# Kernel optimization log

Measured on AMD Instinct MI355X. Metric: run time of the kernel, lower is better.

## Reference

```python
import jax, jax.numpy as jnp
import numpy as np

B, H, P, L = 8, 512, 512, 2048
HIGH_STAB, LOW_STAB = 0.9, 0.99  # 0 <= high < |lambda| <= low <= 1 (discrete dynamics)


def setup_inputs() -> dict:
    key = jax.random.key(0)
    k_u, k_mag, k_ph, k_b, k_c, k_d = jax.random.split(key, 6)
    u = jax.random.normal(k_u, (B, H, L), dtype=jnp.float32)
    # Frozen diagonal reservoir state matrix Lambda_bar: complex eigenvalues with
    # magnitude in (high_stability, low_stability], random phase (stored as real/imag pairs).
    mag = jax.random.uniform(k_mag, (P,), minval=HIGH_STAB, maxval=LOW_STAB)
    phase = jax.random.uniform(k_ph, (P,), minval=0.0, maxval=2.0 * np.pi)
    Lambda_bar_ri = jnp.stack([mag * jnp.cos(phase), mag * jnp.sin(phase)], axis=-1)  # (P,2)
    B_bar_ri = jax.random.normal(k_b, (P, H, 2), dtype=jnp.float32)  # complex B_bar as real pairs
    C_ri = jax.random.normal(k_c, (H, P, 2), dtype=jnp.float32)      # complex C as real pairs
    D = jax.random.normal(k_d, (H, H), dtype=jnp.float32)
    return {"u": u, "Lambda_bar_ri": Lambda_bar_ri, "B_bar_ri": B_bar_ri, "C_ri": C_ri, "D": D}


def _binary_op(e_i, e_j):
    A_i, Bu_i = e_i
    A_j, Bu_j = e_j
    return (A_j * A_i, A_j * Bu_i + Bu_j)


def reference(u, Lambda_bar_ri, B_bar_ri, C_ri, D):
    Lam = jax.lax.complex(Lambda_bar_ri[:, 0], Lambda_bar_ri[:, 1])        # (P,)
    B_bar = jax.lax.complex(B_bar_ri[..., 0], B_bar_ri[..., 1])            # (P,H)
    C = jax.lax.complex(C_ri[..., 0], C_ri[..., 1])                        # (H,P)
    # Bu_t = B_bar @ u_t for all t, batched: (B,P,L) complex
    Bu = jnp.einsum('ph,bhl->bpl', B_bar, u.astype(B_bar.dtype))
    A = jnp.broadcast_to(Lam[None, :, None], Bu.shape)                     # (B,P,L)
    # Parallel associative scan: x_t = Lam * x_{t-1} + Bu_t
    _, x = jax.lax.associative_scan(_binary_op, (A, Bu), axis=2)           # (B,P,L)
    C_A_Bu = jnp.einsum('hp,bpl->bhl', C, x).real                          # (B,H,L)
    # torch.einsum('hh,bhl->bhl', D, u) uses only the diagonal of D
    Du = jnp.diagonal(D)[None, :, None] * u
    return jax.nn.gelu(C_A_Bu + Du, approximate=False)
```

## Files before the change

### kernel.cpp

```cpp
#include <hip/hip_runtime.h>
#include <cstdint>
#include <cstddef>

#define BB 8
#define HH 512
#define PP 512
#define LL 2048

typedef __attribute__((ext_vector_type(8))) __bf16 bf16x8;
typedef __attribute__((ext_vector_type(4))) float f32x4;

__device__ __forceinline__ uint16_t f2bf(float f) {
  uint32_t u = __builtin_bit_cast(uint32_t, f);
  u += 0x7FFFu + ((u >> 16) & 1u);
  return (uint16_t)(u >> 16);
}

__device__ __forceinline__ void async_copy16(const void* gptr, void* ldsptr) {
  __builtin_amdgcn_global_load_lds(
      (const __attribute__((address_space(1))) unsigned int*)gptr,
      (__attribute__((address_space(3))) unsigned int*)ldsptr,
      16, 0, 0);
}

__global__ __launch_bounds__(256) void prep_and_transpose(
    const float* __restrict__ U, const float* __restrict__ Bbar,
    const float* __restrict__ Cri, const float* __restrict__ Dm,
    uint16_t* __restrict__ Ut, uint16_t* __restrict__ A1,
    uint16_t* __restrict__ A2, float* __restrict__ Dd) {
  __shared__ uint16_t tile[64][66];
  const int t = threadIdx.x;
  if (blockIdx.x < 2048) {
    const int bid = blockIdx.x;
    const int b = bid >> 8;
    const int h0 = ((bid >> 5) & 7) * 64;
    const int l0 = (bid & 31) * 64;
    const int r = t >> 2, c = t & 3;
    const float* src = U + ((size_t)(b * 512 + h0 + r)) * 2048 + l0 + c * 16;
#pragma unroll
    for (int q = 0; q < 4; ++q) {
      float4 v = *(const float4*)(src + q * 4);
      *(uint32_t*)&tile[r][c * 16 + q * 4]     = (uint32_t)f2bf(v.x) | ((uint32_t)f2bf(v.y) << 16);
      *(uint32_t*)&tile[r][c * 16 + q * 4 + 2] = (uint32_t)f2bf(v.z) | ((uint32_t)f2bf(v.w) << 16);
    }
    __syncthreads();
    uint16_t* dst = Ut + ((size_t)(b * 2048 + l0 + r)) * 512 + h0 + c * 16;
    uint32_t o[8];
#pragma unroll
    for (int k = 0; k < 8; ++k)
      o[k] = (uint32_t)tile[c * 16 + 2 * k][r] | ((uint32_t)tile[c * 16 + 2 * k + 1][r] << 16);
    *(uint4*)(dst)     = make_uint4(o[0], o[1], o[2], o[3]);
    *(uint4*)(dst + 8) = make_uint4(o[4], o[5], o[6], o[7]);
  } else {
    int idx = (blockIdx.x - 2048) * 256 + t;
    int p = idx >> 9, h = idx & 511;
    A1[(size_t)p * 512 + h]          = f2bf(Bbar[((size_t)p * 512 + h) * 2 + 0]);
    A1[(size_t)(512 + p) * 512 + h]  = f2bf(Bbar[((size_t)p * 512 + h) * 2 + 1]);
    int h2 = idx >> 9, p2 = idx & 511;
    A2[(size_t)h2 * 1024 + p2]        = f2bf( Cri[((size_t)h2 * 512 + p2) * 2 + 0]);
    A2[(size_t)h2 * 1024 + 512 + p2]  = f2bf(-Cri[((size_t)h2 * 512 + p2) * 2 + 1]);
    if (idx < 512) Dd[idx] = Dm[(size_t)idx * 512 + idx];
  }
}

__global__ __launch_bounds__(512) void scan_tr(
    const float* __restrict__ Lam, const uint16_t* __restrict__ Bu,
    uint16_t* __restrict__ Xt8) {
  __shared__ uint16_t S[16][2048];
  const int t = threadIdx.x, wave = t >> 6, lane = t & 63;
  const int b = blockIdx.x >> 6, p0 = (blockIdx.x & 63) * 8, p = p0 + wave;

  const float lr = Lam[p * 2 + 0], li = Lam[p * 2 + 1];
  float ar = lr, ai = li;
#pragma unroll
  for (int s = 0; s < 5; ++s) { float nr = ar * ar - ai * ai, ni = 2.f * ar * ai; ar = nr; ai = ni; }

  const uint16_t* rowre = Bu + ((size_t)(b * 1024 + p)) * 2048 + lane * 32;
  const uint16_t* rowim = Bu + ((size_t)(b * 1024 + 512 + p)) * 2048 + lane * 32;
  uint4 vr[4], vi[4];
#pragma unroll
  for (int q = 0; q < 4; ++q) { vr[q] = ((const uint4*)rowre)[q]; vi[q] = ((const uint4*)rowim)[q]; }

  float xr[32], xi[32];
  float sr = 0.f, si = 0.f;
#pragma unroll
  for (int q = 0; q < 4; ++q) {
    uint32_t wr[4] = {vr[q].x, vr[q].y, vr[q].z, vr[q].w};
    uint32_t wi[4] = {vi[q].x, vi[q].y, vi[q].z, vi[q].w};
#pragma unroll
    for (int d = 0; d < 4; ++d) {
      float br0 = __builtin_bit_cast(float, wr[d] << 16);
      float bi0 = __builtin_bit_cast(float, wi[d] << 16);
      float br1 = __builtin_bit_cast(float, wr[d] & 0xFFFF0000u);
      float bi1 = __builtin_bit_cast(float, wi[d] & 0xFFFF0000u);
      int j = q * 8 + d * 2;
      float nr = lr * sr - li * si + br0, ni = lr * si + li * sr + bi0;
      sr = nr; si = ni; xr[j] = sr; xi[j] = si;
      nr = lr * sr - li * si + br1; ni = lr * si + li * sr + bi1;
      sr = nr; si = ni; xr[j + 1] = sr; xi[j + 1] = si;
    }
  }
  float Ar = ar, Ai = ai, Sr = sr, Si = si;
#pragma unroll
  for (int off = 1; off < 64; off <<= 1) {
    float pAr = __shfl_up(Ar, off), pAi = __shfl_up(Ai, off);
    float pSr = __shfl_up(Sr, off), pSi = __shfl_up(Si, off);
    if (lane >= off) {
      float tSr = Ar * pSr - Ai * pSi + Sr;
      float tSi = Ar * pSi + Ai * pSr + Si;
      float tAr = Ar * pAr - Ai * pAi;
      float tAi = Ar * pAi + Ai * pAr;
      Sr = tSr; Si = tSi; Ar = tAr; Ai = tAi;
    }
  }
  float Cr = __shfl_up(Sr, 1), Ci = __shfl_up(Si, 1);
  if (lane == 0) { Cr = 0.f; Ci = 0.f; }
  float fr_ = lr * Cr - li * Ci, fi_ = lr * Ci + li * Cr;
#pragma unroll
  for (int j = 0; j < 32; ++j) {
    xr[j] += fr_; xi[j] += fi_;
    float nfr = fr_ * lr - fi_ * li, nfi = fr_ * li + fi_ * lr;
    fr_ = nfr; fi_ = nfi;
  }
  const int wsw = (lane & 7) << 3;
#pragma unroll
  for (int q = 0; q < 4; ++q) {
    uint32_t wr[4], wi[4];
#pragma unroll
    for (int d = 0; d < 4; ++d) {
      int j = q * 8 + d * 2;
      wr[d] = (uint32_t)f2bf(xr[j]) | ((uint32_t)f2bf(xr[j + 1]) << 16);
      wi[d] = (uint32_t)f2bf(xi[j]) | ((uint32_t)f2bf(xi[j + 1]) << 16);
    }
    const int col = (lane * 32 + q * 8) ^ wsw;
    *(uint4*)&S[wave * 2 + 0][col] = make_uint4(wr[0], wr[1], wr[2], wr[3]);
    *(uint4*)&S[wave * 2 + 1][col] = make_uint4(wi[0], wi[1], wi[2], wi[3]);
  }
  __syncthreads();
  const size_t gre = (size_t)b * 128 + (p0 >> 3);
#pragma unroll
  for (int c = 0; c < 2; ++c) {
    uint16_t* dst = Xt8 + (gre + (size_t)c * 64) * 2048 * 8;
#pragma unroll
    for (int rep = 0; rep < 4; ++rep) {
      int l = rep * 512 + t;
      int ls = l ^ (((l >> 5) & 7) << 3);
      uint32_t o0 = (uint32_t)S[0 + c][ls] | ((uint32_t)S[2 + c][ls] << 16);
      uint32_t o1 = (uint32_t)S[4 + c][ls] | ((uint32_t)S[6 + c][ls] << 16);
      uint32_t o2 = (uint32_t)S[8 + c][ls] | ((uint32_t)S[10 + c][ls] << 16);
      uint32_t o3 = (uint32_t)S[12 + c][ls] | ((uint32_t)S[14 + c][ls] << 16);
      *(uint4*)(dst + (size_t)l * 8) = make_uint4(o0, o1, o2, o3);
    }
  }
}

#define GEMM_SETUP(KDIM, PB0_EXPR)                                            \
  constexpr int K = (KDIM), NT = K / 32;                                      \
  const int t = threadIdx.x, lane = t & 63, w = t >> 6;                       \
  const int m0 = blockIdx.y * 128, n0 = blockIdx.x * 64, b = blockIdx.z;      \
  const int r0 = t >> 2;                                                      \
  const int c0 = (t & 3) ^ ((r0 >> 1) & 3);                                   \
  const uint16_t* pA0 = Amat + (size_t)(m0 + r0) * K + c0 * 8;                \
  const uint16_t* pA1 = Amat + (size_t)(m0 + 64 + r0) * K + c0 * 8;           \
  const uint16_t* pB0 = (PB0_EXPR);                                           \
  const int d0 = t * 8;                                                       \
  const int wm = (w >> 1) * 64, wn = (w & 1) * 32;                            \
  const int fr = lane & 15, fq = lane >> 4;                                   \
  int offA[4], offB[2];                                                       \
  _Pragma("unroll")                                                           \
  for (int i = 0; i < 4; ++i) {                                               \
    int rm = wm + i * 16 + fr;                                                \
    offA[i] = rm * 32 + ((fq ^ ((rm >> 1) & 3)) * 8);                         \
  }                                                                           \
  _Pragma("unroll")                                                           \
  for (int j = 0; j < 2; ++j) {                                               \
    int rn = wn + j * 16 + fr;                                                \
    offB[j] = rn * 32 + ((fq ^ ((rn >> 1) & 3)) * 8);                         \
  }                                                                           \
  f32x4 acc[4][2];                                                            \
  _Pragma("unroll")                                                           \
  for (int i = 0; i < 4; ++i)                                                 \
    _Pragma("unroll")                                                         \
    for (int j = 0; j < 2; ++j) acc[i][j] = (f32x4){0.f, 0.f, 0.f, 0.f};

#define GEMM_MFMA_BLOCK(BUF_A, BUF_B)                                         \
  {                                                                           \
    bf16x8 af[4], bv[2];                                                      \
    _Pragma("unroll")                                                         \
    for (int i = 0; i < 4; ++i) af[i] = *(const bf16x8*)&(BUF_A)[offA[i]];    \
    _Pragma("unroll")                                                         \
    for (int j = 0; j < 2; ++j) bv[j] = *(const bf16x8*)&(BUF_B)[offB[j]];    \
    _Pragma("unroll")                                                         \
    for (int i = 0; i < 4; ++i)                                               \
      _Pragma("unroll")                                                       \
      for (int j = 0; j < 2; ++j)                                             \
        acc[i][j] = __builtin_amdgcn_mfma_f32_16x16x32_bf16(af[i], bv[j], acc[i][j], 0, 0, 0); \
  }

__global__ __launch_bounds__(256) void gemm1_fused(
    const uint16_t* __restrict__ Amat, const uint16_t* __restrict__ Bt,
    uint16_t* __restrict__ Bu) {
  __shared__ __align__(16) uint16_t Alds[2][128 * 32];
  __shared__ __align__(16) uint16_t Blds[2][64 * 32];
  GEMM_SETUP(512, Bt + ((size_t)b * 2048 + n0 + r0) * 512 + c0 * 8)
  async_copy16(pA0, &Alds[0][d0]);
  async_copy16(pA1, &Alds[0][2048 + d0]);
  async_copy16(pB0, &Blds[0][d0]);
  __syncthreads();
#pragma unroll 2
  for (int it = 0; it < NT; ++it) {
    const int cur = it & 1, nxt = cur ^ 1;
    if (it + 1 < NT) {
      const int kb = (it + 1) * 32;
      async_copy16(pA0 + kb, &Alds[nxt][d0]);
      async_copy16(pA1 + kb, &Alds[nxt][2048 + d0]);
      async_copy16(pB0 + kb, &Blds[nxt][d0]);
    }
    GEMM_MFMA_BLOCK(Alds[cur], Blds[cur])
    __syncthreads();
  }
  uint16_t* O = Bu + ((size_t)b * 1024 + m0) * 2048 + n0;
#pragma unroll
  for (int i = 0; i < 4; ++i)
#pragma unroll
    for (int j = 0; j < 2; ++j)
#pragma unroll
      for (int r = 0; r < 4; ++r) {
        int mm = wm + i * 16 + fq * 4 + r;
        int nn = wn + j * 16 + fr;
        O[(size_t)mm * 2048 + nn] = f2bf(acc[i][j][r]);
      }
}

__global__ __launch_bounds__(256) void gemm2_fused(
    const uint16_t* __restrict__ Amat, const uint16_t* __restrict__ Bt,
    float* __restrict__ Out, const float* __restrict__ Dd,
    const float* __restrict__ Uu) {
  __shared__ __align__(16) uint16_t Alds[3][128 * 32];
  __shared__ __align__(16) uint16_t Blds[3][64 * 32];
  GEMM_SETUP(1024, Bt + (((size_t)b * 128 + c0) * 2048 + n0 + r0) * 8)
  constexpr size_t BSTRIDE = 65536;
  async_copy16(pA0,           &Alds[0][d0]);
  async_copy16(pA1,           &Alds[0][2048 + d0]);
  async_copy16(pB0,           &Blds[0][d0]);
  async_copy16(pA0 + 32,      &Alds[1][d0]);
  async_copy16(pA1 + 32,      &Alds[1][2048 + d0]);
  async_copy16(pB0 + BSTRIDE, &Blds[1][d0]);
#pragma unroll
  for (int kt = 0; kt < NT; ++kt) {
    const int cur = kt % 3;
    if (kt + 1 < NT) asm volatile("s_waitcnt vmcnt(3)" ::: "memory");
    else             asm volatile("s_waitcnt vmcnt(0)" ::: "memory");
    __builtin_amdgcn_s_barrier();
    __builtin_amdgcn_sched_barrier(0);
    if (kt + 2 < NT) {
      const int nb = (kt + 2) % 3;
      const int kb = (kt + 2) * 32;
      async_copy16(pA0 + kb, &Alds[nb][d0]);
      async_copy16(pA1 + kb, &Alds[nb][2048 + d0]);
      async_copy16(pB0 + (size_t)(kt + 2) * BSTRIDE, &Blds[nb][d0]);
    }
    GEMM_MFMA_BLOCK(Alds[cur], Blds[cur])
  }
  const size_t base = ((size_t)b * 512 + m0) * 2048 + n0;
  float* O = Out + base;
  const float* Ub = Uu + base;
#pragma unroll
  for (int i = 0; i < 4; ++i)
#pragma unroll
    for (int r = 0; r < 4; ++r) {
      int mm = wm + i * 16 + fq * 4 + r;
      float dv = Dd[m0 + mm];
#pragma unroll
      for (int j = 0; j < 2; ++j) {
        int nn = wn + j * 16 + fr;
        float xv = acc[i][j][r] + dv * Ub[(size_t)mm * 2048 + nn];
        O[(size_t)mm * 2048 + nn] = 0.5f * xv * (1.f + erff(xv * 0.70710678118654752f));
      }
    }
}

extern "C" void kernel_launch(void* const* d_in, const int* in_sizes, int n_in,
                              void* d_out, int out_size, void* d_ws, size_t ws_size,
                              hipStream_t stream) {
  const float* u    = (const float*)d_in[0];
  const float* Lam  = (const float*)d_in[1];
  const float* Bbar = (const float*)d_in[2];
  const float* Cri  = (const float*)d_in[3];
  const float* Dm   = (const float*)d_in[4];
  float* out = (float*)d_out;

  char* ws = (char*)d_ws;
  uint16_t* Bu  = (uint16_t*)(ws);
  uint16_t* Xt8 = (uint16_t*)(ws + 33554432);
  uint16_t* Ut  = (uint16_t*)(ws + 33554432);
  uint16_t* A1 = (uint16_t*)(ws + 67108864);
  uint16_t* A2 = (uint16_t*)(ws + 68157440);
  float*    Dd = (float*)   (ws + 69206016);

  prep_and_transpose<<<3072, 256, 0, stream>>>(u, Bbar, Cri, Dm, Ut, A1, A2, Dd);
  gemm1_fused<<<dim3(32, 8, BB), 256, 0, stream>>>(A1, Ut, Bu);
  scan_tr<<<512, 512, 0, stream>>>(Lam, Bu, Xt8);
  gemm2_fused<<<dim3(32, 4, BB), 256, 0, stream>>>(A2, Xt8, out, Dd, u);
}
```

Baseline: 174.4 us.

## Fuse u transpose and bf16 conversion into gemm1 B-tile loading

Removes the separate transpose kernel that converted u to a bf16 (B,L,H) buffer. gemm1 now reads fp32 u directly with float4 loads, converts it to bf16 and writes it into the swizzled B tile in LDS, so the intermediate Ut write and read are gone. The cost is synchronous global loads plus conversion inside the main loop in place of async LDS copies, and u is reread for each of the 8 M-blocks.

```diff
diff --git a/kernel.cpp b/kernel.cpp
--- a/kernel.cpp
+++ b/kernel.cpp
@@ -23,44 +23,19 @@
       16, 0, 0);
 }
 
-__global__ __launch_bounds__(256) void prep_and_transpose(
-    const float* __restrict__ U, const float* __restrict__ Bbar,
-    const float* __restrict__ Cri, const float* __restrict__ Dm,
-    uint16_t* __restrict__ Ut, uint16_t* __restrict__ A1,
-    uint16_t* __restrict__ A2, float* __restrict__ Dd) {
-  __shared__ uint16_t tile[64][66];
-  const int t = threadIdx.x;
-  if (blockIdx.x < 2048) {
-    const int bid = blockIdx.x;
-    const int b = bid >> 8;
-    const int h0 = ((bid >> 5) & 7) * 64;
-    const int l0 = (bid & 31) * 64;
-    const int r = t >> 2, c = t & 3;
-    const float* src = U + ((size_t)(b * 512 + h0 + r)) * 2048 + l0 + c * 16;
-#pragma unroll
-    for (int q = 0; q < 4; ++q) {
-      float4 v = *(const float4*)(src + q * 4);
-      *(uint32_t*)&tile[r][c * 16 + q * 4]     = (uint32_t)f2bf(v.x) | ((uint32_t)f2bf(v.y) << 16);
-      *(uint32_t*)&tile[r][c * 16 + q * 4 + 2] = (uint32_t)f2bf(v.z) | ((uint32_t)f2bf(v.w) << 16);
-    }
-    __syncthreads();
-    uint16_t* dst = Ut + ((size_t)(b * 2048 + l0 + r)) * 512 + h0 + c * 16;
-    uint32_t o[8];
-#pragma unroll
-    for (int k = 0; k < 8; ++k)
-      o[k] = (uint32_t)tile[c * 16 + 2 * k][r] | ((uint32_t)tile[c * 16 + 2 * k + 1][r] << 16);
-    *(uint4*)(dst)     = make_uint4(o[0], o[1], o[2], o[3]);
-    *(uint4*)(dst + 8) = make_uint4(o[4], o[5], o[6], o[7]);
-  } else {
-    int idx = (blockIdx.x - 2048) * 256 + t;
-    int p = idx >> 9, h = idx & 511;
-    A1[(size_t)p * 512 + h]          = f2bf(Bbar[((size_t)p * 512 + h) * 2 + 0]);
-    A1[(size_t)(512 + p) * 512 + h]  = f2bf(Bbar[((size_t)p * 512 + h) * 2 + 1]);
-    int h2 = idx >> 9, p2 = idx & 511;
-    A2[(size_t)h2 * 1024 + p2]        = f2bf( Cri[((size_t)h2 * 512 + p2) * 2 + 0]);
-    A2[(size_t)h2 * 1024 + 512 + p2]  = f2bf(-Cri[((size_t)h2 * 512 + p2) * 2 + 1]);
-    if (idx < 512) Dd[idx] = Dm[(size_t)idx * 512 + idx];
-  }
+__global__ __launch_bounds__(256) void prep_mats(
+    const float* __restrict__ Bbar, const float* __restrict__ Cri,
+    const float* __restrict__ Dm,
+    uint16_t* __restrict__ A1, uint16_t* __restrict__ A2,
+    float* __restrict__ Dd) {
+  int idx = blockIdx.x * 256 + threadIdx.x;
+  int p = idx >> 9, h = idx & 511;
+  A1[(size_t)p * 512 + h]          = f2bf(Bbar[((size_t)p * 512 + h) * 2 + 0]);
+  A1[(size_t)(512 + p) * 512 + h]  = f2bf(Bbar[((size_t)p * 512 + h) * 2 + 1]);
+  int h2 = idx >> 9, p2 = idx & 511;
+  A2[(size_t)h2 * 1024 + p2]        = f2bf( Cri[((size_t)h2 * 512 + p2) * 2 + 0]);
+  A2[(size_t)h2 * 1024 + 512 + p2]  = f2bf(-Cri[((size_t)h2 * 512 + p2) * 2 + 1]);
+  if (idx < 512) Dd[idx] = Dm[(size_t)idx * 512 + idx];
 }
 
 __global__ __launch_bounds__(512) void scan_tr(
@@ -153,35 +128,6 @@
     }
   }
 }
-
-#define GEMM_SETUP(KDIM, PB0_EXPR)                                            \
-  constexpr int K = (KDIM), NT = K / 32;                                      \
-  const int t = threadIdx.x, lane = t & 63, w = t >> 6;                       \
-  const int m0 = blockIdx.y * 128, n0 = blockIdx.x * 64, b = blockIdx.z;      \
-  const int r0 = t >> 2;                                                      \
-  const int c0 = (t & 3) ^ ((r0 >> 1) & 3);                                   \
-  const uint16_t* pA0 = Amat + (size_t)(m0 + r0) * K + c0 * 8;                \
-  const uint16_t* pA1 = Amat + (size_t)(m0 + 64 + r0) * K + c0 * 8;           \
-  const uint16_t* pB0 = (PB0_EXPR);                                           \
-  const int d0 = t * 8;                                                       \
-  const int wm = (w >> 1) * 64, wn = (w & 1) * 32;                            \
-  const int fr = lane & 15, fq = lane >> 4;                                   \
-  int offA[4], offB[2];                                                       \
-  _Pragma("unroll")                                                           \
-  for (int i = 0; i < 4; ++i) {                                               \
-    int rm = wm + i * 16 + fr;                                                \
-    offA[i] = rm * 32 + ((fq ^ ((rm >> 1) & 3)) * 8);                         \
-  }                                                                           \
-  _Pragma("unroll")                                                           \
-  for (int j = 0; j < 2; ++j) {                                               \
-    int rn = wn + j * 16 + fr;                                                \
-    offB[j] = rn * 32 + ((fq ^ ((rn >> 1) & 3)) * 8);                         \
-  }                                                                           \
-  f32x4 acc[4][2];                                                            \
-  _Pragma("unroll")                                                           \
-  for (int i = 0; i < 4; ++i)                                                 \
-    _Pragma("unroll")                                                         \
-    for (int j = 0; j < 2; ++j) acc[i][j] = (f32x4){0.f, 0.f, 0.f, 0.f};
 
 #define GEMM_MFMA_BLOCK(BUF_A, BUF_B)                                         \
   {                                                                           \
@@ -198,15 +144,59 @@
   }
 
 __global__ __launch_bounds__(256) void gemm1_fused(
-    const uint16_t* __restrict__ Amat, const uint16_t* __restrict__ Bt,
+    const uint16_t* __restrict__ Amat, const float* __restrict__ U,
     uint16_t* __restrict__ Bu) {
+  constexpr int K = 512, NT = K / 32;
   __shared__ __align__(16) uint16_t Alds[2][128 * 32];
   __shared__ __align__(16) uint16_t Blds[2][64 * 32];
-  GEMM_SETUP(512, Bt + ((size_t)b * 2048 + n0 + r0) * 512 + c0 * 8)
+  const int t = threadIdx.x, lane = t & 63, w = t >> 6;
+  const int m0 = blockIdx.y * 128, n0 = blockIdx.x * 64, b = blockIdx.z;
+  const int r0 = t >> 2;
+  const int c0 = (t & 3) ^ ((r0 >> 1) & 3);
+  const uint16_t* pA0 = Amat + (size_t)(m0 + r0) * K + c0 * 8;
+  const uint16_t* pA1 = Amat + (size_t)(m0 + 64 + r0) * K + c0 * 8;
+  const int d0 = t * 8;
+  const int a = t >> 4, lq = t & 15;
+  const float* pu = U + ((size_t)(b * 512) + 2 * a) * 2048 + n0 + lq * 4;
+  int offW[4];
+#pragma unroll
+  for (int i = 0; i < 4; ++i) {
+    int l = lq * 4 + i;
+    offW[i] = l * 32 + (((a >> 2) ^ ((l >> 1) & 3)) << 3) + ((a & 3) << 1);
+  }
+  const int wm = (w >> 1) * 64, wn = (w & 1) * 32;
+  const int fr = lane & 15, fq = lane >> 4;
+  int offA[4], offB[2];
+#pragma unroll
+  for (int i = 0; i < 4; ++i) {
+    int rm = wm + i * 16 + fr;
+    offA[i] = rm * 32 + ((fq ^ ((rm >> 1) & 3)) * 8);
+  }
+#pragma unroll
+  for (int j = 0; j < 2; ++j) {
+    int rn = wn + j * 16 + fr;
+    offB[j] = rn * 32 + ((fq ^ ((rn >> 1) & 3)) * 8);
+  }
+  f32x4 acc[4][2];
+#pragma unroll
+  for (int i = 0; i < 4; ++i)
+#pragma unroll
+    for (int j = 0; j < 2; ++j) acc[i][j] = (f32x4){0.f, 0.f, 0.f, 0.f};
+
   async_copy16(pA0, &Alds[0][d0]);
   async_copy16(pA1, &Alds[0][2048 + d0]);
-  async_copy16(pB0, &Blds[0][d0]);
+  {
+    float4 v0 = *(const float4*)(pu);
+    float4 v1 = *(const float4*)(pu + 2048);
+    float r0a[4] = {v0.x, v0.y, v0.z, v0.w};
+    float r1a[4] = {v1.x, v1.y, v1.z, v1.w};
+#pragma unroll
+    for (int i = 0; i < 4; ++i)
+      *(uint32_t*)&Blds[0][offW[i]] =
+          (uint32_t)f2bf(r0a[i]) | ((uint32_t)f2bf(r1a[i]) << 16);
+  }
   __syncthreads();
+
 #pragma unroll 2
   for (int it = 0; it < NT; ++it) {
     const int cur = it & 1, nxt = cur ^ 1;
@@ -214,7 +204,15 @@
       const int kb = (it + 1) * 32;
       async_copy16(pA0 + kb, &Alds[nxt][d0]);
       async_copy16(pA1 + kb, &Alds[nxt][2048 + d0]);
-      async_copy16(pB0 + kb, &Blds[nxt][d0]);
+      const float* s = pu + (size_t)kb * 2048;
+      float4 v0 = *(const float4*)(s);
+      float4 v1 = *(const float4*)(s + 2048);
+      float r0a[4] = {v0.x, v0.y, v0.z, v0.w};
+      float r1a[4] = {v1.x, v1.y, v1.z, v1.w};
+#pragma unroll
+      for (int i = 0; i < 4; ++i)
+        *(uint32_t*)&Blds[nxt][offW[i]] =
+            (uint32_t)f2bf(r0a[i]) | ((uint32_t)f2bf(r1a[i]) << 16);
     }
     GEMM_MFMA_BLOCK(Alds[cur], Blds[cur])
     __syncthreads();
@@ -236,9 +234,35 @@
     const uint16_t* __restrict__ Amat, const uint16_t* __restrict__ Bt,
     float* __restrict__ Out, const float* __restrict__ Dd,
     const float* __restrict__ Uu) {
+  constexpr int K = 1024, NT = K / 32;
   __shared__ __align__(16) uint16_t Alds[3][128 * 32];
   __shared__ __align__(16) uint16_t Blds[3][64 * 32];
-  GEMM_SETUP(1024, Bt + (((size_t)b * 128 + c0) * 2048 + n0 + r0) * 8)
+  const int t = threadIdx.x, lane = t & 63, w = t >> 6;
+  const int m0 = blockIdx.y * 128, n0 = blockIdx.x * 64, b = blockIdx.z;
+  const int r0 = t >> 2;
+  const int c0 = (t & 3) ^ ((r0 >> 1) & 3);
+  const uint16_t* pA0 = Amat + (size_t)(m0 + r0) * K + c0 * 8;
+  const uint16_t* pA1 = Amat + (size_t)(m0 + 64 + r0) * K + c0 * 8;
+  const uint16_t* pB0 = Bt + (((size_t)b * 128 + c0) * 2048 + n0 + r0) * 8;
+  const int d0 = t * 8;
+  const int wm = (w >> 1) * 64, wn = (w & 1) * 32;
+  const int fr = lane & 15, fq = lane >> 4;
+  int offA[4], offB[2];
+#pragma unroll
+  for (int i = 0; i < 4; ++i) {
+    int rm = wm + i * 16 + fr;
+    offA[i] = rm * 32 + ((fq ^ ((rm >> 1) & 3)) * 8);
+  }
+#pragma unroll
+  for (int j = 0; j < 2; ++j) {
+    int rn = wn + j * 16 + fr;
+    offB[j] = rn * 32 + ((fq ^ ((rn >> 1) & 3)) * 8);
+  }
+  f32x4 acc[4][2];
+#pragma unroll
+  for (int i = 0; i < 4; ++i)
+#pragma unroll
+    for (int j = 0; j < 2; ++j) acc[i][j] = (f32x4){0.f, 0.f, 0.f, 0.f};
   constexpr size_t BSTRIDE = 65536;
   async_copy16(pA0,           &Alds[0][d0]);
   async_copy16(pA1,           &Alds[0][2048 + d0]);
@@ -293,13 +317,12 @@
   char* ws = (char*)d_ws;
   uint16_t* Bu  = (uint16_t*)(ws);
   uint16_t* Xt8 = (uint16_t*)(ws + 33554432);
-  uint16_t* Ut  = (uint16_t*)(ws + 33554432);
   uint16_t* A1 = (uint16_t*)(ws + 67108864);
   uint16_t* A2 = (uint16_t*)(ws + 68157440);
   float*    Dd = (float*)   (ws + 69206016);
 
-  prep_and_transpose<<<3072, 256, 0, stream>>>(u, Bbar, Cri, Dm, Ut, A1, A2, Dd);
-  gemm1_fused<<<dim3(32, 8, BB), 256, 0, stream>>>(A1, Ut, Bu);
+  prep_mats<<<1024, 256, 0, stream>>>(Bbar, Cri, Dm, A1, A2, Dd);
+  gemm1_fused<<<dim3(32, 8, BB), 256, 0, stream>>>(A1, u, Bu);
   scan_tr<<<512, 512, 0, stream>>>(Lam, Bu, Xt8);
   gemm2_fused<<<dim3(32, 4, BB), 256, 0, stream>>>(A2, Xt8, out, Dd, u);
 }
```

New measurement: 182.4 us. +4.6%, slower.
